# Performance work log

Hardware: AMD Instinct MI355X
Metric: run time of the kernel (lower is better)

## Reference

```python
import jax, jax.numpy as jnp
import numpy as np

EPS = 1e-12
NEG = -1e30


def setup_inputs() -> dict:
    key = jax.random.key(0)
    ks = jax.random.split(key, 7)
    B, Nq, Lp, H, D = 96, 35, 180, 768, 128
    q_hidden = jax.random.normal(ks[0], (B, Nq, H), dtype=jnp.float32)
    pos_hidden = jax.random.normal(ks[1], (B, Lp, H), dtype=jnp.float32)
    neg_hidden = jax.random.normal(ks[2], (B, Lp, H), dtype=jnp.float32)
    W = jax.random.normal(ks[3], (H, D), dtype=jnp.float32) * 0.02
    b = jax.random.normal(ks[4], (D,), dtype=jnp.float32) * 0.02
    # non-punctuation filter mask; guarantee at least one valid token per passage
    pos_mask = jax.random.bernoulli(ks[5], 0.85, (B, Lp)).at[:, 0].set(True)
    neg_mask = jax.random.bernoulli(ks[6], 0.85, (B, Lp)).at[:, 0].set(True)
    return {"q_hidden": q_hidden, "pos_hidden": pos_hidden, "neg_hidden": neg_hidden,
            "W": W, "b": b, "pos_mask": pos_mask, "neg_mask": neg_mask}


def _vector_representation(h, W, b):
    # Linear projection then F.normalize(x) with torch default dim=1,
    # i.e. normalization over the SEQUENCE axis (faithful to source).
    x = jnp.einsum('blh,hd->bld', h, W) + b
    norm = jnp.maximum(jnp.sqrt(jnp.sum(x * x, axis=1, keepdims=True)), EPS)
    return x / norm


def _late_interaction(q, p, mask):
    # q: [Bq, Nq, D], p: [Bp, Lp, D], mask: [Bp, Lp] (True = keep token)
    sim = jnp.einsum('qnd,pld->qpnl', q, p)          # [Bq, Bp, Nq, Lp]
    sim = jnp.where(mask[None, :, None, :], sim, NEG)
    return jnp.max(sim, axis=-1).sum(axis=-1)        # MaxSim: max over Lp, sum over Nq


def reference(q_hidden, pos_hidden, neg_hidden, W, b, pos_mask, neg_mask):
    q = _vector_representation(q_hidden, W, b)
    pos = _vector_representation(pos_hidden, W, b)
    neg = _vector_representation(neg_hidden, W, b)
    pos_scores = _late_interaction(q, pos, pos_mask)
    neg_scores = _late_interaction(q, neg, neg_mask)
    return jnp.concatenate((pos_scores, neg_scores), axis=1)  # [B, 2B]
```

## Files before the change

### kernel.cpp

```cpp
#include <hip/hip_runtime.h>

typedef __attribute__((ext_vector_type(4))) float f32x4;
typedef __attribute__((ext_vector_type(8))) short s16x8;
typedef __attribute__((ext_vector_type(4))) short s16x4;
typedef __bf16 bf16x4 __attribute__((ext_vector_type(4)));

#define B_   96
#define NQ   35
#define LP   180
#define H_   768
#define D_   128
#define NEGF (-1e30f)

#define NROWS 37920
#define QROWS 3360
#define PROWS 17280

__device__ __forceinline__ unsigned short f2bf(float f) {
    return __builtin_bit_cast(unsigned short, (__bf16)f);
}

__device__ __forceinline__ s16x4 cvt_bf4(f32x4 v) {
    return __builtin_bit_cast(s16x4, __builtin_convertvector(v, bf16x4));
}

__device__ __forceinline__ s16x8 pack_bf16(f32x4 v0, f32x4 v1) {
    bf16x4 h0 = __builtin_convertvector(v0, bf16x4);
    bf16x4 h1 = __builtin_convertvector(v1, bf16x4);
    s16x4 a = __builtin_bit_cast(s16x4, h0), b = __builtin_bit_cast(s16x4, h1);
    return __builtin_shufflevector(a, b, 0, 1, 2, 3, 4, 5, 6, 7);
}

__device__ __forceinline__ void glds16(const void* g, void* l) {
    __builtin_amdgcn_global_load_lds(
        (const __attribute__((address_space(1))) unsigned int*)g,
        (__attribute__((address_space(3))) unsigned int*)l,
        16, 0, 0);
}

__device__ __forceinline__ s16x8 ldg16(const unsigned short* sbase, unsigned int voff) {
    s16x8 r;
    asm volatile("global_load_dwordx4 %0, %1, %2"
                 : "=v"(r) : "v"(voff), "s"(sbase));
    return r;
}

#define WAITV(N) do {                                                 \
    asm volatile("s_waitcnt vmcnt(" #N ")" ::: "memory");             \
    __builtin_amdgcn_sched_barrier(0);                                \
} while (0)

#define BAR() do {                                                    \
    __builtin_amdgcn_sched_barrier(0);                                \
    __builtin_amdgcn_s_barrier();                                     \
} while (0)

__global__ __launch_bounds__(256) void prep_k(
    const float* __restrict__ W, unsigned short* __restrict__ wthi,
    const unsigned int* __restrict__ pmask_w, unsigned int* __restrict__ ctrl,
    float* __restrict__ ssq) {
    __shared__ unsigned int rr[256];
    int b = blockIdx.x, t = threadIdx.x;
    if (b < 48) {
        int tid = b * 256 + t;
        int nt = tid / (24 * 64);
        int r = tid - nt * 24 * 64;
        int ks = r / 64, lane = r - ks * 64;
        int m = lane & 15, quad = lane >> 4;
        unsigned short* o = wthi + (size_t)tid * 8;
#pragma unroll
        for (int j = 0; j < 8; j++) {
            int k = ks * 32 + quad * 8 + j;
            o[j] = f2bf(W[(size_t)k * D_ + nt * 16 + m]);
        }
    } else if (b < 192) {
        ssq[(b - 48) * 256 + t] = 0.f;
    } else {
        unsigned int f1 = 0, f3 = 0, f4 = 0;
        for (int w = t; w < 4320; w += 256) {
            unsigned int v = pmask_w[w];
            f1 |= v & 0x0000ff00u;
            f3 |= v & 0xff000000u;
            if (w & 1) f4 |= v & 0x000000ffu;
        }
        rr[t] = f1; __syncthreads();
        for (int s2 = 128; s2; s2 >>= 1) { if (t < s2) rr[t] |= rr[t + s2]; __syncthreads(); }
        if (!t) ctrl[0] = rr[0];
        __syncthreads();
        rr[t] = f3; __syncthreads();
        for (int s2 = 128; s2; s2 >>= 1) { if (t < s2) rr[t] |= rr[t + s2]; __syncthreads(); }
        if (!t) ctrl[1] = rr[0];
        __syncthreads();
        rr[t] = f4; __syncthreads();
        for (int s2 = 128; s2; s2 >>= 1) { if (t < s2) rr[t] |= rr[t + s2]; __syncthreads(); }
        if (!t) ctrl[2] = rr[0];
    }
}

#define STAGE(S) do {                                                                     \
    float* ldw = ld0 + ((S)&3) * 2048;                                                    \
    glds16(gq0 + (S) * 64, ldw);                                                          \
    glds16(gq1 + (S) * 64, ldw + 256);                                                    \
} while (0)

#define LDB(p0, p1, p2, p3, S1) do {                                                      \
    unsigned int k0 = (unsigned int)((S1) * 2048u);                                       \
    p0 = ldg16(wthi, ob0 + k0);                                                           \
    p1 = ldg16(wthi, ob1 + k0);                                                           \
    p2 = ldg16(wthi, ob0 + k0 + 1024u);                                                   \
    p3 = ldg16(wthi, ob1 + k0 + 1024u);                                                   \
} while (0)

#define ACOMP(S, B0, B1, B2, B3) do {                                                     \
    const float* bb = &lds[((S)&3) * 2048];                                               \
    f32x4 l, h;                                                                           \
    l = *(const f32x4*)(bb + rb0 + cA0); h = *(const f32x4*)(bb + rb0 + cA0 + 4);         \
    s16x8 a00 = pack_bf16(l, h);                                                          \
    l = *(const f32x4*)(bb + rb1 + cA0); h = *(const f32x4*)(bb + rb1 + cA0 + 4);         \
    s16x8 a10 = pack_bf16(l, h);                                                          \
    l = *(const f32x4*)(bb + rb0 + cA1); h = *(const f32x4*)(bb + rb0 + cA1 + 4);         \
    s16x8 a01 = pack_bf16(l, h);                                                          \
    l = *(const f32x4*)(bb + rb1 + cA1); h = *(const f32x4*)(bb + rb1 + cA1 + 4);         \
    s16x8 a11 = pack_bf16(l, h);                                                          \
    acc[0][0] = __builtin_amdgcn_mfma_f32_16x16x32_bf16(a00, B0, acc[0][0], 0, 0, 0);     \
    acc[0][1] = __builtin_amdgcn_mfma_f32_16x16x32_bf16(a00, B1, acc[0][1], 0, 0, 0);     \
    acc[1][0] = __builtin_amdgcn_mfma_f32_16x16x32_bf16(a10, B0, acc[1][0], 0, 0, 0);     \
    acc[1][1] = __builtin_amdgcn_mfma_f32_16x16x32_bf16(a10, B1, acc[1][1], 0, 0, 0);     \
    acc[0][0] = __builtin_amdgcn_mfma_f32_16x16x32_bf16(a01, B2, acc[0][0], 0, 0, 0);     \
    acc[0][1] = __builtin_amdgcn_mfma_f32_16x16x32_bf16(a01, B3, acc[0][1], 0, 0, 0);     \
    acc[1][0] = __builtin_amdgcn_mfma_f32_16x16x32_bf16(a11, B2, acc[1][0], 0, 0, 0);     \
    acc[1][1] = __builtin_amdgcn_mfma_f32_16x16x32_bf16(a11, B3, acc[1][1], 0, 0, 0);     \
} while (0)

__global__ __launch_bounds__(256, 4) void proj_k(
    const float* __restrict__ qh, const float* __restrict__ ph, const float* __restrict__ nh,
    const unsigned short* __restrict__ wthi, const float* __restrict__ bias,
    float* __restrict__ x, float* __restrict__ ssq,
    const void* __restrict__ pm, const void* __restrict__ nm,
    const unsigned int* __restrict__ ctrl, unsigned char* __restrict__ maskc) {
    __shared__ float lds[8192];
    int b = blockIdx.x;
    if (b >= 1185) {
        int i = (b - 1185) * 256 + threadIdx.x;
        const void* src = (i < B_ * LP) ? pm : nm;
        int j = (i < B_ * LP) ? i : i - B_ * LP;
        unsigned int c1 = ctrl[0], c3 = ctrl[1], c4 = ctrl[2];
        bool bit;
        if (c1 > 0)       bit = ((const unsigned char*)src)[j] != 0;
        else if (c3 > 0)  bit = ((const float*)src)[j] != 0.0f;
        else if (c4 > 0)  bit = ((const int*)src)[j] != 0;
        else              bit = ((const long long*)src)[j] != 0;
        maskc[i] = bit ? 1 : 0;
        return;
    }
    int t = threadIdx.x;
    int wave = t >> 6, lane = t & 63;
    const float* src; int row0l; int growbase;
    if (b < 105)      { src = qh; row0l = b * 32;         growbase = row0l; }
    else if (b < 645) { src = ph; row0l = (b - 105) * 32; growbase = QROWS + row0l; }
    else              { src = nh; row0l = (b - 645) * 32; growbase = QROWS + PROWS + row0l; }
    int m = lane & 15, quad = lane >> 4;

    int r0 = wave * 8 + (lane >> 4);
    int r1 = r0 + 4;
    int cg0 = (lane & 15) ^ (2 * (r0 & 7));
    int cg1 = (lane & 15) ^ (2 * (r1 & 7));
    const float* gq0 = src + (size_t)(row0l + r0) * H_ + cg0 * 4;
    const float* gq1 = src + (size_t)(row0l + r1) * H_ + cg1 * 4;
    float* ld0 = &lds[wave * 512];

    int nt0 = wave * 2, nt1 = wave * 2 + 1;
    unsigned int ob0 = (unsigned int)(((nt0 * 24) * 64 + lane) * 16);
    unsigned int ob1 = (unsigned int)(((nt1 * 24) * 64 + lane) * 16);

    int swz = 2 * (m & 7);
    int rb0 = m * 64, rb1 = (m + 16) * 64;
    int cA0 = ((quad * 2) ^ swz) * 4;
    int cA1 = ((8 + quad * 2) ^ swz) * 4;

    f32x4 acc[2][2];
#pragma unroll
    for (int mt = 0; mt < 2; mt++)
#pragma unroll
        for (int ntl = 0; ntl < 2; ntl++) acc[mt][ntl] = (f32x4){0.f, 0.f, 0.f, 0.f};

    s16x8 bA0, bA1, bA2, bA3, bB0, bB1, bB2, bB3;

    STAGE(0);
    STAGE(1);
    LDB(bA0, bA1, bA2, bA3, 0);
    STAGE(2);
    WAITV(8);

    BAR(); LDB(bB0, bB1, bB2, bB3, 1);  STAGE(3);  WAITV(8); ACOMP(0,  bA0, bA1, bA2, bA3);
    BAR(); LDB(bA0, bA1, bA2, bA3, 2);  STAGE(4);  WAITV(8); ACOMP(1,  bB0, bB1, bB2, bB3);
    BAR(); LDB(bB0, bB1, bB2, bB3, 3);  STAGE(5);  WAITV(8); ACOMP(2,  bA0, bA1, bA2, bA3);
    BAR(); LDB(bA0, bA1, bA2, bA3, 4);  STAGE(6);  WAITV(8); ACOMP(3,  bB0, bB1, bB2, bB3);
    BAR(); LDB(bB0, bB1, bB2, bB3, 5);  STAGE(7);  WAITV(8); ACOMP(4,  bA0, bA1, bA2, bA3);
    BAR(); LDB(bA0, bA1, bA2, bA3, 6);  STAGE(8);  WAITV(8); ACOMP(5,  bB0, bB1, bB2, bB3);
    BAR(); LDB(bB0, bB1, bB2, bB3, 7);  STAGE(9);  WAITV(8); ACOMP(6,  bA0, bA1, bA2, bA3);
    BAR(); LDB(bA0, bA1, bA2, bA3, 8);  STAGE(10); WAITV(8); ACOMP(7,  bB0, bB1, bB2, bB3);
    BAR(); LDB(bB0, bB1, bB2, bB3, 9);  STAGE(11); WAITV(8); ACOMP(8,  bA0, bA1, bA2, bA3);
    BAR(); LDB(bA0, bA1, bA2, bA3, 10);            WAITV(6); ACOMP(9,  bB0, bB1, bB2, bB3);
    BAR(); LDB(bB0, bB1, bB2, bB3, 11);            WAITV(4); ACOMP(10, bA0, bA1, bA2, bA3);
    BAR();                                         WAITV(0); ACOMP(11, bB0, bB1, bB2, bB3);

#pragma unroll
    for (int mt = 0; mt < 2; mt++) {
        int base = growbase + mt * 16;
        int bk0, bk1, b1start;
        if (base < QROWS)              { bk0 = base / 35;  bk1 = (base + 15) / 35;
                                         b1start = bk1 * 35; }
        else if (base < QROWS + PROWS) { int r0e = base - QROWS;
                                         bk0 = 96 + r0e / 180;  bk1 = 96 + (r0e + 15) / 180;
                                         b1start = QROWS + (bk1 - 96) * 180; }
        else                           { int r0e = base - QROWS - PROWS;
                                         bk0 = 192 + r0e / 180; bk1 = 192 + (r0e + 15) / 180;
                                         b1start = QROWS + PROWS + (bk1 - 192) * 180; }
#pragma unroll
        for (int ntl = 0; ntl < 2; ntl++) {
            int col = (wave * 2 + ntl) * 16 + m;
            float bv = bias[col];
            f32x4 s4 = acc[mt][ntl];
            float slo = 0.f, shi = 0.f;
#pragma unroll
            for (int r = 0; r < 4; r++) {
                int grow = base + quad * 4 + r;
                float v = s4[r] + bv;
                x[(size_t)grow * D_ + col] = v;
                float v2 = v * v;
                if (bk1 > bk0 && grow >= b1start) shi += v2; else slo += v2;
            }
            slo += __shfl_xor(slo, 16); slo += __shfl_xor(slo, 32);
            if (quad == 0) atomicAdd(ssq + (size_t)bk0 * D_ + col, slo);
            if (bk1 > bk0) {
                shi += __shfl_xor(shi, 16); shi += __shfl_xor(shi, 32);
                if (quad == 0) atomicAdd(ssq + (size_t)bk1 * D_ + col, shi);
            }
        }
    }
}

__global__ __launch_bounds__(256) void scatter_k(
    const float* __restrict__ x, const float* __restrict__ ssq,
    const unsigned char* __restrict__ maskc,
    unsigned short* __restrict__ qfrag, unsigned short* __restrict__ pfrag) {
    int c = blockIdx.x * 256 + threadIdx.x;
    int lane = c & 63, ks = (c >> 6) & 3;
    int quad = lane >> 4, mm = lane & 15;
    int d0 = ks * 32 + quad * 8;
    if (c < 61440) {
        int g = c >> 8;
        int mt = g % 5, qp = g / 5;
        int prow = mt * 16 + mm;
        s16x8 outv = (s16x8){0, 0, 0, 0, 0, 0, 0, 0};
        if (prow < 70) {
            int hi = prow >= 35;
            int bq = qp * 2 + hi;
            int l = prow - hi * 35;
            size_t row = (size_t)bq * 35 + l;
            const f32x4* px = (const f32x4*)(x + row * D_ + d0);
            f32x4 v0 = px[0], v1 = px[1];
            const f32x4* pq = (const f32x4*)(ssq + (size_t)bq * D_ + d0);
            f32x4 q0 = pq[0], q1 = pq[1];
            f32x4 r0, r1;
#pragma unroll
            for (int j = 0; j < 4; j++) {
                r0[j] = rsqrtf(fmaxf(q0[j], 1e-24f));
                r1[j] = rsqrtf(fmaxf(q1[j], 1e-24f));
            }
            outv = pack_bf16(v0 * r0, v1 * r1);
        }
        *(s16x8*)(qfrag + (size_t)c * 8) = outv;
    } else {
        int c2 = c - 61440;
        int g = c2 >> 8;
        int nt = g % 12, pbk = g / 12;
        int l = nt * 16 + mm;
        int lsrc = (l < LP && maskc[pbk * LP + l]) ? l : 0;
        size_t row = QROWS + (size_t)pbk * LP + lsrc;
        const f32x4* px = (const f32x4*)(x + row * D_ + d0);
        f32x4 v0 = px[0], v1 = px[1];
        const f32x4* pq = (const f32x4*)(ssq + (size_t)(96 + pbk) * D_ + d0);
        f32x4 q0 = pq[0], q1 = pq[1];
        f32x4 r0, r1;
#pragma unroll
        for (int j = 0; j < 4; j++) {
            r0[j] = rsqrtf(fmaxf(q0[j], 1e-24f));
            r1[j] = rsqrtf(fmaxf(q1[j], 1e-24f));
        }
        *(s16x8*)(pfrag + (size_t)c2 * 8) = pack_bf16(v0 * r0, v1 * r1);
    }
}

__global__ __launch_bounds__(256, 3) void interact_k(
    const unsigned short* __restrict__ qfrag, const unsigned short* __restrict__ pfrag,
    float* __restrict__ out) {
    __shared__ unsigned short plds[24576];
    int wave = threadIdx.x >> 6, lane = threadIdx.x & 63;
    int b = blockIdx.x;
    int xcd = b & 7, i = b >> 3;
    int c = xcd * 24 + (i % 24);
    int qg = i / 24;
    int side = c / 96, pb = c - side * 96;
    int qp = qg * 4 + wave;
    int m = lane & 15, quad = lane >> 4;

    const unsigned short* pbase = pfrag + (size_t)c * 24576;
    const unsigned short* qbase = qfrag + (size_t)qp * 10240;

#pragma unroll
    for (int ntl = 0; ntl < 3; ntl++) {
        int nt = wave * 3 + ntl;
#pragma unroll
        for (int ks = 0; ks < 4; ks++)
            glds16(pbase + ((size_t)(nt * 4 + ks) * 64 + lane) * 8,
                   &plds[(size_t)(nt * 4 + ks) * 512]);
    }

    s16x8 a[5][4];
#pragma unroll
    for (int mt = 0; mt < 5; mt++)
#pragma unroll
        for (int ks = 0; ks < 4; ks++)
            a[mt][ks] = *(const s16x8*)(qbase + ((size_t)(mt * 4 + ks) * 64 + lane) * 8);

    __syncthreads();

    const f32x4 zero4 = (f32x4){0.f, 0.f, 0.f, 0.f};
    float rmax[5][4];
#pragma unroll
    for (int mt = 0; mt < 5; mt++)
#pragma unroll
        for (int rr = 0; rr < 4; rr++) rmax[mt][rr] = NEGF;

    for (int nt = 0; nt < 12; nt++) {
        s16x8 bfr[4];
#pragma unroll
        for (int ks = 0; ks < 4; ks++)
            bfr[ks] = *(const s16x8*)&plds[((size_t)(nt * 4 + ks) * 64 + lane) * 8];
#pragma unroll
        for (int mt = 0; mt < 5; mt++) {
            f32x4 acc = __builtin_amdgcn_mfma_f32_16x16x32_bf16(a[mt][0], bfr[0], zero4, 0, 0, 0);
            acc = __builtin_amdgcn_mfma_f32_16x16x32_bf16(a[mt][1], bfr[1], acc, 0, 0, 0);
            acc = __builtin_amdgcn_mfma_f32_16x16x32_bf16(a[mt][2], bfr[2], acc, 0, 0, 0);
            acc = __builtin_amdgcn_mfma_f32_16x16x32_bf16(a[mt][3], bfr[3], acc, 0, 0, 0);
#pragma unroll
            for (int rr = 0; rr < 4; rr++)
                rmax[mt][rr] = fmaxf(rmax[mt][rr], acc[rr]);
        }
    }

#pragma unroll
    for (int mt = 0; mt < 5; mt++)
#pragma unroll
        for (int rr = 0; rr < 4; rr++) {
            float v = rmax[mt][rr];
            v = fmaxf(v, __shfl_xor(v, 1));
            v = fmaxf(v, __shfl_xor(v, 2));
            v = fmaxf(v, __shfl_xor(v, 4));
            v = fmaxf(v, __shfl_xor(v, 8));
            rmax[mt][rr] = v;
        }
    float s0 = 0.f, s1 = 0.f;
#pragma unroll
    for (int mt = 0; mt < 5; mt++)
#pragma unroll
        for (int rr = 0; rr < 4; rr++) {
            int prow = mt * 16 + quad * 4 + rr;
            float v = rmax[mt][rr];
            if (prow < 35) s0 += v;
            else if (prow < 70) s1 += v;
        }
    s0 += __shfl_xor(s0, 16); s0 += __shfl_xor(s0, 32);
    s1 += __shfl_xor(s1, 16); s1 += __shfl_xor(s1, 32);
    if (lane == 0) {
        int qb0 = qp * 2, qb1 = qp * 2 + 1;
        out[(size_t)qb0 * (2 * B_) + side * B_ + pb] = s0;
        out[(size_t)qb1 * (2 * B_) + side * B_ + pb] = s1;
    }
}

extern "C" void kernel_launch(void* const* d_in, const int* in_sizes, int n_in,
                              void* d_out, int out_size, void* d_ws, size_t ws_size,
                              hipStream_t stream) {
    const float* qh   = (const float*)d_in[0];
    const float* ph   = (const float*)d_in[1];
    const float* nh   = (const float*)d_in[2];
    const float* W    = (const float*)d_in[3];
    const float* bias = (const float*)d_in[4];
    const void* pmask = d_in[5];
    const void* nmask = d_in[6];
    float* out = (float*)d_out;
    char* ws = (char*)d_ws;

    constexpr size_t CTRL_OFF  = 0;
    constexpr size_t WTHI_OFF  = 256;
    constexpr size_t MASKC_OFF = WTHI_OFF + 196608;
    constexpr size_t SSQ_OFF   = 231424;
    constexpr size_t X_OFF     = SSQ_OFF + 147456;
    constexpr size_t QFRAG_OFF = X_OFF + (size_t)NROWS * D_ * 4;
    constexpr size_t PFRAG_OFF = QFRAG_OFF + 983040;

    unsigned int* ctrl     = (unsigned int*)(ws + CTRL_OFF);
    unsigned short* wthi   = (unsigned short*)(ws + WTHI_OFF);
    unsigned char* maskc   = (unsigned char*)(ws + MASKC_OFF);
    float* ssq             = (float*)(ws + SSQ_OFF);
    float* x               = (float*)(ws + X_OFF);
    unsigned short* qfrag  = (unsigned short*)(ws + QFRAG_OFF);
    unsigned short* pfrag  = (unsigned short*)(ws + PFRAG_OFF);

    prep_k<<<193, 256, 0, stream>>>(W, wthi, (const unsigned int*)pmask, ctrl, ssq);
    proj_k<<<1185 + 135, 256, 0, stream>>>(qh, ph, nh, wthi, bias, x, ssq,
                                           pmask, nmask, ctrl, maskc);
    scatter_k<<<2544, 256, 0, stream>>>(x, ssq, maskc, qfrag, pfrag);
    interact_k<<<2304, 256, 0, stream>>>(qfrag, pfrag, out);
}
```

Baseline: 197.5 us.

## Restructure projection GEMM pipeline into two four-stage LDS buffers with fewer barriers

Replaces the per-stage four-slot LDS ring, which needed a barrier every k-step, with two large buffers that each hold four k-stages. The buffers are filled in bulk, and a three-deep register rotation of weight fragments prefetches further ahead. The aim is to cut barrier count from twelve to three and to hide more global latency. In exchange, LDS per block doubles and launch bounds drop to two blocks per CU, which lowers occupancy.

```diff
diff --git a/kernel.cpp b/kernel.cpp
--- a/kernel.cpp
+++ b/kernel.cpp
@@ -97,10 +97,16 @@
     }
 }
 
-#define STAGE(S) do {                                                                     \
-    float* ldw = ld0 + ((S)&3) * 2048;                                                    \
-    glds16(gq0 + (S) * 64, ldw);                                                          \
-    glds16(gq1 + (S) * 64, ldw + 256);                                                    \
+#define STAGEG(BUF, S0) do {                                                              \
+    float* dst = ld0 + (BUF) * 8192;                                                      \
+    glds16(gq0 + ((S0) + 0) * 64, dst);                                                   \
+    glds16(gq1 + ((S0) + 0) * 64, dst + 256);                                             \
+    glds16(gq0 + ((S0) + 1) * 64, dst + 2048);                                            \
+    glds16(gq1 + ((S0) + 1) * 64, dst + 2304);                                            \
+    glds16(gq0 + ((S0) + 2) * 64, dst + 4096);                                            \
+    glds16(gq1 + ((S0) + 2) * 64, dst + 4352);                                            \
+    glds16(gq0 + ((S0) + 3) * 64, dst + 6144);                                            \
+    glds16(gq1 + ((S0) + 3) * 64, dst + 6400);                                            \
 } while (0)
 
 #define LDB(p0, p1, p2, p3, S1) do {                                                      \
@@ -111,8 +117,8 @@
     p3 = ldg16(wthi, ob1 + k0 + 1024u);                                                   \
 } while (0)
 
-#define ACOMP(S, B0, B1, B2, B3) do {                                                     \
-    const float* bb = &lds[((S)&3) * 2048];                                               \
+#define ACOMP(S, BUF, B0, B1, B2, B3) do {                                                \
+    const float* bb = &lds[(BUF) * 8192 + ((S)&3) * 2048];                                \
     f32x4 l, h;                                                                           \
     l = *(const f32x4*)(bb + rb0 + cA0); h = *(const f32x4*)(bb + rb0 + cA0 + 4);         \
     s16x8 a00 = pack_bf16(l, h);                                                          \
@@ -132,13 +138,13 @@
     acc[1][1] = __builtin_amdgcn_mfma_f32_16x16x32_bf16(a11, B3, acc[1][1], 0, 0, 0);     \
 } while (0)
 
-__global__ __launch_bounds__(256, 4) void proj_k(
+__global__ __launch_bounds__(256, 2) void proj_k(
     const float* __restrict__ qh, const float* __restrict__ ph, const float* __restrict__ nh,
     const unsigned short* __restrict__ wthi, const float* __restrict__ bias,
     float* __restrict__ x, float* __restrict__ ssq,
     const void* __restrict__ pm, const void* __restrict__ nm,
     const unsigned int* __restrict__ ctrl, unsigned char* __restrict__ maskc) {
-    __shared__ float lds[8192];
+    __shared__ float lds[16384];
     int b = blockIdx.x;
     if (b >= 1185) {
         int i = (b - 1185) * 256 + threadIdx.x;
@@ -184,26 +190,32 @@
 #pragma unroll
         for (int ntl = 0; ntl < 2; ntl++) acc[mt][ntl] = (f32x4){0.f, 0.f, 0.f, 0.f};
 
-    s16x8 bA0, bA1, bA2, bA3, bB0, bB1, bB2, bB3;
-
-    STAGE(0);
-    STAGE(1);
-    LDB(bA0, bA1, bA2, bA3, 0);
-    STAGE(2);
-    WAITV(8);
-
-    BAR(); LDB(bB0, bB1, bB2, bB3, 1);  STAGE(3);  WAITV(8); ACOMP(0,  bA0, bA1, bA2, bA3);
-    BAR(); LDB(bA0, bA1, bA2, bA3, 2);  STAGE(4);  WAITV(8); ACOMP(1,  bB0, bB1, bB2, bB3);
-    BAR(); LDB(bB0, bB1, bB2, bB3, 3);  STAGE(5);  WAITV(8); ACOMP(2,  bA0, bA1, bA2, bA3);
-    BAR(); LDB(bA0, bA1, bA2, bA3, 4);  STAGE(6);  WAITV(8); ACOMP(3,  bB0, bB1, bB2, bB3);
-    BAR(); LDB(bB0, bB1, bB2, bB3, 5);  STAGE(7);  WAITV(8); ACOMP(4,  bA0, bA1, bA2, bA3);
-    BAR(); LDB(bA0, bA1, bA2, bA3, 6);  STAGE(8);  WAITV(8); ACOMP(5,  bB0, bB1, bB2, bB3);
-    BAR(); LDB(bB0, bB1, bB2, bB3, 7);  STAGE(9);  WAITV(8); ACOMP(6,  bA0, bA1, bA2, bA3);
-    BAR(); LDB(bA0, bA1, bA2, bA3, 8);  STAGE(10); WAITV(8); ACOMP(7,  bB0, bB1, bB2, bB3);
-    BAR(); LDB(bB0, bB1, bB2, bB3, 9);  STAGE(11); WAITV(8); ACOMP(8,  bA0, bA1, bA2, bA3);
-    BAR(); LDB(bA0, bA1, bA2, bA3, 10);            WAITV(6); ACOMP(9,  bB0, bB1, bB2, bB3);
-    BAR(); LDB(bB0, bB1, bB2, bB3, 11);            WAITV(4); ACOMP(10, bA0, bA1, bA2, bA3);
-    BAR();                                         WAITV(0); ACOMP(11, bB0, bB1, bB2, bB3);
+    s16x8 sa0, sa1, sa2, sa3;
+    s16x8 sb0, sb1, sb2, sb3;
+    s16x8 sc0, sc1, sc2, sc3;
+
+    STAGEG(0, 0);
+    LDB(sa0, sa1, sa2, sa3, 0);
+    LDB(sb0, sb1, sb2, sb3, 1);
+    STAGEG(1, 4);
+    LDB(sc0, sc1, sc2, sc3, 2);
+
+    WAITV(16); BAR();
+    ACOMP(0, 0, sa0, sa1, sa2, sa3);
+    LDB(sa0, sa1, sa2, sa3, 3);  WAITV(16); ACOMP(1, 0, sb0, sb1, sb2, sb3);
+    LDB(sb0, sb1, sb2, sb3, 4);  WAITV(8);  ACOMP(2, 0, sc0, sc1, sc2, sc3);
+    LDB(sc0, sc1, sc2, sc3, 5);  WAITV(8);  ACOMP(3, 0, sa0, sa1, sa2, sa3);
+    BAR();
+    STAGEG(0, 8);
+    LDB(sa0, sa1, sa2, sa3, 6);  WAITV(16); ACOMP(4, 1, sb0, sb1, sb2, sb3);
+    LDB(sb0, sb1, sb2, sb3, 7);  WAITV(16); ACOMP(5, 1, sc0, sc1, sc2, sc3);
+    LDB(sc0, sc1, sc2, sc3, 8);  WAITV(8);  ACOMP(6, 1, sa0, sa1, sa2, sa3);
+    LDB(sa0, sa1, sa2, sa3, 9);  WAITV(8);  ACOMP(7, 1, sb0, sb1, sb2, sb3);
+    BAR();
+    LDB(sb0, sb1, sb2, sb3, 10); WAITV(8);  ACOMP(8, 0, sc0, sc1, sc2, sc3);
+    LDB(sc0, sc1, sc2, sc3, 11); WAITV(8);  ACOMP(9, 0, sa0, sa1, sa2, sa3);
+    WAITV(4);  ACOMP(10, 0, sb0, sb1, sb2, sb3);
+    WAITV(0);  ACOMP(11, 0, sc0, sc1, sc2, sc3);
 
 #pragma unroll
     for (int mt = 0; mt < 2; mt++) {
```

After: 197.8 us. Within noise of the previous version (+0.2%).

## Enlarge projection tile to 64 rows with triple-buffered LDS pipeline

Applied to the files above, without the earlier changes.

The projection GEMM now gives each block 64 rows instead of 32, and lets a block span the query, positive and negative inputs through a per-row source selector with a clamped tail. The main aim is to halve the per-row reloads of the bf16 weight fragments from global memory and L2. LDS staging moves from a 4-stage to a 3-stage ring of larger buffers, and B fragments rotate through three register sets. In exchange, per-block LDS use and accumulator registers grow, occupancy drops from 4 to 3 blocks, and the last block is only half full.

```diff
diff --git a/kernel.cpp b/kernel.cpp
--- a/kernel.cpp
+++ b/kernel.cpp
@@ -54,6 +54,16 @@
     __builtin_amdgcn_sched_barrier(0);                                \
     __builtin_amdgcn_s_barrier();                                     \
 } while (0)
+
+__device__ __forceinline__ const float* rowsrc(const float* qh, const float* ph,
+                                               const float* nh, int r, int lane) {
+    int rc = r < (NROWS - 1) ? r : (NROWS - 1);
+    const float* p;
+    if (rc < QROWS)              p = qh + (size_t)rc * H_;
+    else if (rc < QROWS + PROWS) p = ph + (size_t)(rc - QROWS) * H_;
+    else                         p = nh + (size_t)(rc - QROWS - PROWS) * H_;
+    return p + (((lane & 15) ^ (2 * (rc & 7))) << 2);
+}
 
 __global__ __launch_bounds__(256) void prep_k(
     const float* __restrict__ W, unsigned short* __restrict__ wthi,
@@ -97,10 +107,12 @@
     }
 }
 
-#define STAGE(S) do {                                                                     \
-    float* ldw = ld0 + ((S)&3) * 2048;                                                    \
-    glds16(gq0 + (S) * 64, ldw);                                                          \
-    glds16(gq1 + (S) * 64, ldw + 256);                                                    \
+#define STAGE64(S) do {                                                                   \
+    float* dst = &lds[((S) % 3) * 4096 + wave * 1024];                                    \
+    glds16(gq0 + (S) * 64, dst);                                                          \
+    glds16(gq1 + (S) * 64, dst + 256);                                                    \
+    glds16(gq2 + (S) * 64, dst + 512);                                                    \
+    glds16(gq3 + (S) * 64, dst + 768);                                                    \
 } while (0)
 
 #define LDB(p0, p1, p2, p3, S1) do {                                                      \
@@ -111,37 +123,53 @@
     p3 = ldg16(wthi, ob1 + k0 + 1024u);                                                   \
 } while (0)
 
-#define ACOMP(S, B0, B1, B2, B3) do {                                                     \
-    const float* bb = &lds[((S)&3) * 2048];                                               \
-    f32x4 l, h;                                                                           \
-    l = *(const f32x4*)(bb + rb0 + cA0); h = *(const f32x4*)(bb + rb0 + cA0 + 4);         \
-    s16x8 a00 = pack_bf16(l, h);                                                          \
-    l = *(const f32x4*)(bb + rb1 + cA0); h = *(const f32x4*)(bb + rb1 + cA0 + 4);         \
-    s16x8 a10 = pack_bf16(l, h);                                                          \
-    l = *(const f32x4*)(bb + rb0 + cA1); h = *(const f32x4*)(bb + rb0 + cA1 + 4);         \
-    s16x8 a01 = pack_bf16(l, h);                                                          \
-    l = *(const f32x4*)(bb + rb1 + cA1); h = *(const f32x4*)(bb + rb1 + cA1 + 4);         \
-    s16x8 a11 = pack_bf16(l, h);                                                          \
-    acc[0][0] = __builtin_amdgcn_mfma_f32_16x16x32_bf16(a00, B0, acc[0][0], 0, 0, 0);     \
-    acc[0][1] = __builtin_amdgcn_mfma_f32_16x16x32_bf16(a00, B1, acc[0][1], 0, 0, 0);     \
-    acc[1][0] = __builtin_amdgcn_mfma_f32_16x16x32_bf16(a10, B0, acc[1][0], 0, 0, 0);     \
-    acc[1][1] = __builtin_amdgcn_mfma_f32_16x16x32_bf16(a10, B1, acc[1][1], 0, 0, 0);     \
-    acc[0][0] = __builtin_amdgcn_mfma_f32_16x16x32_bf16(a01, B2, acc[0][0], 0, 0, 0);     \
-    acc[0][1] = __builtin_amdgcn_mfma_f32_16x16x32_bf16(a01, B3, acc[0][1], 0, 0, 0);     \
-    acc[1][0] = __builtin_amdgcn_mfma_f32_16x16x32_bf16(a11, B2, acc[1][0], 0, 0, 0);     \
-    acc[1][1] = __builtin_amdgcn_mfma_f32_16x16x32_bf16(a11, B3, acc[1][1], 0, 0, 0);     \
+#define ACOMP64(S, B0, B1, B2, B3) do {                                                   \
+    const float* bb = &lds[((S) % 3) * 4096];                                             \
+    f32x4 l, h; s16x8 a0, a1, a2, a3;                                                     \
+    l = *(const f32x4*)(bb + rbm0 + cA0); h = *(const f32x4*)(bb + rbm0 + cA0 + 4);       \
+    a0 = pack_bf16(l, h);                                                                 \
+    l = *(const f32x4*)(bb + rbm1 + cA0); h = *(const f32x4*)(bb + rbm1 + cA0 + 4);       \
+    a1 = pack_bf16(l, h);                                                                 \
+    l = *(const f32x4*)(bb + rbm2 + cA0); h = *(const f32x4*)(bb + rbm2 + cA0 + 4);       \
+    a2 = pack_bf16(l, h);                                                                 \
+    l = *(const f32x4*)(bb + rbm3 + cA0); h = *(const f32x4*)(bb + rbm3 + cA0 + 4);       \
+    a3 = pack_bf16(l, h);                                                                 \
+    acc[0][0] = __builtin_amdgcn_mfma_f32_16x16x32_bf16(a0, B0, acc[0][0], 0, 0, 0);      \
+    acc[0][1] = __builtin_amdgcn_mfma_f32_16x16x32_bf16(a0, B1, acc[0][1], 0, 0, 0);      \
+    acc[1][0] = __builtin_amdgcn_mfma_f32_16x16x32_bf16(a1, B0, acc[1][0], 0, 0, 0);      \
+    acc[1][1] = __builtin_amdgcn_mfma_f32_16x16x32_bf16(a1, B1, acc[1][1], 0, 0, 0);      \
+    acc[2][0] = __builtin_amdgcn_mfma_f32_16x16x32_bf16(a2, B0, acc[2][0], 0, 0, 0);      \
+    acc[2][1] = __builtin_amdgcn_mfma_f32_16x16x32_bf16(a2, B1, acc[2][1], 0, 0, 0);      \
+    acc[3][0] = __builtin_amdgcn_mfma_f32_16x16x32_bf16(a3, B0, acc[3][0], 0, 0, 0);      \
+    acc[3][1] = __builtin_amdgcn_mfma_f32_16x16x32_bf16(a3, B1, acc[3][1], 0, 0, 0);      \
+    l = *(const f32x4*)(bb + rbm0 + cA1); h = *(const f32x4*)(bb + rbm0 + cA1 + 4);       \
+    a0 = pack_bf16(l, h);                                                                 \
+    l = *(const f32x4*)(bb + rbm1 + cA1); h = *(const f32x4*)(bb + rbm1 + cA1 + 4);       \
+    a1 = pack_bf16(l, h);                                                                 \
+    l = *(const f32x4*)(bb + rbm2 + cA1); h = *(const f32x4*)(bb + rbm2 + cA1 + 4);       \
+    a2 = pack_bf16(l, h);                                                                 \
+    l = *(const f32x4*)(bb + rbm3 + cA1); h = *(const f32x4*)(bb + rbm3 + cA1 + 4);       \
+    a3 = pack_bf16(l, h);                                                                 \
+    acc[0][0] = __builtin_amdgcn_mfma_f32_16x16x32_bf16(a0, B2, acc[0][0], 0, 0, 0);      \
+    acc[0][1] = __builtin_amdgcn_mfma_f32_16x16x32_bf16(a0, B3, acc[0][1], 0, 0, 0);      \
+    acc[1][0] = __builtin_amdgcn_mfma_f32_16x16x32_bf16(a1, B2, acc[1][0], 0, 0, 0);      \
+    acc[1][1] = __builtin_amdgcn_mfma_f32_16x16x32_bf16(a1, B3, acc[1][1], 0, 0, 0);      \
+    acc[2][0] = __builtin_amdgcn_mfma_f32_16x16x32_bf16(a2, B2, acc[2][0], 0, 0, 0);      \
+    acc[2][1] = __builtin_amdgcn_mfma_f32_16x16x32_bf16(a2, B3, acc[2][1], 0, 0, 0);      \
+    acc[3][0] = __builtin_amdgcn_mfma_f32_16x16x32_bf16(a3, B2, acc[3][0], 0, 0, 0);      \
+    acc[3][1] = __builtin_amdgcn_mfma_f32_16x16x32_bf16(a3, B3, acc[3][1], 0, 0, 0);      \
 } while (0)
 
-__global__ __launch_bounds__(256, 4) void proj_k(
+__global__ __launch_bounds__(256, 3) void proj_k(
     const float* __restrict__ qh, const float* __restrict__ ph, const float* __restrict__ nh,
     const unsigned short* __restrict__ wthi, const float* __restrict__ bias,
     float* __restrict__ x, float* __restrict__ ssq,
     const void* __restrict__ pm, const void* __restrict__ nm,
     const unsigned int* __restrict__ ctrl, unsigned char* __restrict__ maskc) {
-    __shared__ float lds[8192];
+    __shared__ float lds[12288];
     int b = blockIdx.x;
-    if (b >= 1185) {
-        int i = (b - 1185) * 256 + threadIdx.x;
+    if (b >= 593) {
+        int i = (b - 593) * 256 + threadIdx.x;
         const void* src = (i < B_ * LP) ? pm : nm;
         int j = (i < B_ * LP) ? i : i - B_ * LP;
         unsigned int c1 = ctrl[0], c3 = ctrl[1], c4 = ctrl[2];
@@ -155,87 +183,83 @@
     }
     int t = threadIdx.x;
     int wave = t >> 6, lane = t & 63;
-    const float* src; int row0l; int growbase;
-    if (b < 105)      { src = qh; row0l = b * 32;         growbase = row0l; }
-    else if (b < 645) { src = ph; row0l = (b - 105) * 32; growbase = QROWS + row0l; }
-    else              { src = nh; row0l = (b - 645) * 32; growbase = QROWS + PROWS + row0l; }
+    int row0 = b * 64;
     int m = lane & 15, quad = lane >> 4;
 
-    int r0 = wave * 8 + (lane >> 4);
-    int r1 = r0 + 4;
-    int cg0 = (lane & 15) ^ (2 * (r0 & 7));
-    int cg1 = (lane & 15) ^ (2 * (r1 & 7));
-    const float* gq0 = src + (size_t)(row0l + r0) * H_ + cg0 * 4;
-    const float* gq1 = src + (size_t)(row0l + r1) * H_ + cg1 * 4;
-    float* ld0 = &lds[wave * 512];
+    int rbase = row0 + wave * 16 + (lane >> 4);
+    const float* gq0 = rowsrc(qh, ph, nh, rbase,      lane);
+    const float* gq1 = rowsrc(qh, ph, nh, rbase + 4,  lane);
+    const float* gq2 = rowsrc(qh, ph, nh, rbase + 8,  lane);
+    const float* gq3 = rowsrc(qh, ph, nh, rbase + 12, lane);
 
     int nt0 = wave * 2, nt1 = wave * 2 + 1;
     unsigned int ob0 = (unsigned int)(((nt0 * 24) * 64 + lane) * 16);
     unsigned int ob1 = (unsigned int)(((nt1 * 24) * 64 + lane) * 16);
 
     int swz = 2 * (m & 7);
-    int rb0 = m * 64, rb1 = (m + 16) * 64;
+    int rbm0 = m * 64, rbm1 = rbm0 + 1024, rbm2 = rbm0 + 2048, rbm3 = rbm0 + 3072;
     int cA0 = ((quad * 2) ^ swz) * 4;
     int cA1 = ((8 + quad * 2) ^ swz) * 4;
 
-    f32x4 acc[2][2];
-#pragma unroll
-    for (int mt = 0; mt < 2; mt++)
+    f32x4 acc[4][2];
+#pragma unroll
+    for (int mt = 0; mt < 4; mt++)
 #pragma unroll
         for (int ntl = 0; ntl < 2; ntl++) acc[mt][ntl] = (f32x4){0.f, 0.f, 0.f, 0.f};
 
-    s16x8 bA0, bA1, bA2, bA3, bB0, bB1, bB2, bB3;
-
-    STAGE(0);
-    STAGE(1);
-    LDB(bA0, bA1, bA2, bA3, 0);
-    STAGE(2);
-    WAITV(8);
-
-    BAR(); LDB(bB0, bB1, bB2, bB3, 1);  STAGE(3);  WAITV(8); ACOMP(0,  bA0, bA1, bA2, bA3);
-    BAR(); LDB(bA0, bA1, bA2, bA3, 2);  STAGE(4);  WAITV(8); ACOMP(1,  bB0, bB1, bB2, bB3);
-    BAR(); LDB(bB0, bB1, bB2, bB3, 3);  STAGE(5);  WAITV(8); ACOMP(2,  bA0, bA1, bA2, bA3);
-    BAR(); LDB(bA0, bA1, bA2, bA3, 4);  STAGE(6);  WAITV(8); ACOMP(3,  bB0, bB1, bB2, bB3);
-    BAR(); LDB(bB0, bB1, bB2, bB3, 5);  STAGE(7);  WAITV(8); ACOMP(4,  bA0, bA1, bA2, bA3);
-    BAR(); LDB(bA0, bA1, bA2, bA3, 6);  STAGE(8);  WAITV(8); ACOMP(5,  bB0, bB1, bB2, bB3);
-    BAR(); LDB(bB0, bB1, bB2, bB3, 7);  STAGE(9);  WAITV(8); ACOMP(6,  bA0, bA1, bA2, bA3);
-    BAR(); LDB(bA0, bA1, bA2, bA3, 8);  STAGE(10); WAITV(8); ACOMP(7,  bB0, bB1, bB2, bB3);
-    BAR(); LDB(bB0, bB1, bB2, bB3, 9);  STAGE(11); WAITV(8); ACOMP(8,  bA0, bA1, bA2, bA3);
-    BAR(); LDB(bA0, bA1, bA2, bA3, 10);            WAITV(6); ACOMP(9,  bB0, bB1, bB2, bB3);
-    BAR(); LDB(bB0, bB1, bB2, bB3, 11);            WAITV(4); ACOMP(10, bA0, bA1, bA2, bA3);
-    BAR();                                         WAITV(0); ACOMP(11, bB0, bB1, bB2, bB3);
-
-#pragma unroll
-    for (int mt = 0; mt < 2; mt++) {
-        int base = growbase + mt * 16;
-        int bk0, bk1, b1start;
-        if (base < QROWS)              { bk0 = base / 35;  bk1 = (base + 15) / 35;
-                                         b1start = bk1 * 35; }
-        else if (base < QROWS + PROWS) { int r0e = base - QROWS;
-                                         bk0 = 96 + r0e / 180;  bk1 = 96 + (r0e + 15) / 180;
-                                         b1start = QROWS + (bk1 - 96) * 180; }
-        else                           { int r0e = base - QROWS - PROWS;
-                                         bk0 = 192 + r0e / 180; bk1 = 192 + (r0e + 15) / 180;
-                                         b1start = QROWS + PROWS + (bk1 - 192) * 180; }
-#pragma unroll
-        for (int ntl = 0; ntl < 2; ntl++) {
-            int col = (wave * 2 + ntl) * 16 + m;
-            float bv = bias[col];
-            f32x4 s4 = acc[mt][ntl];
-            float slo = 0.f, shi = 0.f;
-#pragma unroll
-            for (int r = 0; r < 4; r++) {
-                int grow = base + quad * 4 + r;
-                float v = s4[r] + bv;
-                x[(size_t)grow * D_ + col] = v;
-                float v2 = v * v;
-                if (bk1 > bk0 && grow >= b1start) shi += v2; else slo += v2;
-            }
-            slo += __shfl_xor(slo, 16); slo += __shfl_xor(slo, 32);
-            if (quad == 0) atomicAdd(ssq + (size_t)bk0 * D_ + col, slo);
-            if (bk1 > bk0) {
-                shi += __shfl_xor(shi, 16); shi += __shfl_xor(shi, 32);
-                if (quad == 0) atomicAdd(ssq + (size_t)bk1 * D_ + col, shi);
+    s16x8 sa0, sa1, sa2, sa3;
+    s16x8 sb0, sb1, sb2, sb3;
+    s16x8 sc0, sc1, sc2, sc3;
+
+    STAGE64(0); LDB(sa0, sa1, sa2, sa3, 0);
+    STAGE64(1); LDB(sb0, sb1, sb2, sb3, 1);
+
+    WAITV(8); BAR(); STAGE64(2);  LDB(sc0, sc1, sc2, sc3, 2);  ACOMP64(0,  sa0, sa1, sa2, sa3);
+    WAITV(8); BAR(); STAGE64(3);  LDB(sa0, sa1, sa2, sa3, 3);  ACOMP64(1,  sb0, sb1, sb2, sb3);
+    WAITV(8); BAR(); STAGE64(4);  LDB(sb0, sb1, sb2, sb3, 4);  ACOMP64(2,  sc0, sc1, sc2, sc3);
+    WAITV(8); BAR(); STAGE64(5);  LDB(sc0, sc1, sc2, sc3, 5);  ACOMP64(3,  sa0, sa1, sa2, sa3);
+    WAITV(8); BAR(); STAGE64(6);  LDB(sa0, sa1, sa2, sa3, 6);  ACOMP64(4,  sb0, sb1, sb2, sb3);
+    WAITV(8); BAR(); STAGE64(7);  LDB(sb0, sb1, sb2, sb3, 7);  ACOMP64(5,  sc0, sc1, sc2, sc3);
+    WAITV(8); BAR(); STAGE64(8);  LDB(sc0, sc1, sc2, sc3, 8);  ACOMP64(6,  sa0, sa1, sa2, sa3);
+    WAITV(8); BAR(); STAGE64(9);  LDB(sa0, sa1, sa2, sa3, 9);  ACOMP64(7,  sb0, sb1, sb2, sb3);
+    WAITV(8); BAR(); STAGE64(10); LDB(sb0, sb1, sb2, sb3, 10); ACOMP64(8,  sc0, sc1, sc2, sc3);
+    WAITV(8); BAR(); STAGE64(11); LDB(sc0, sc1, sc2, sc3, 11); ACOMP64(9,  sa0, sa1, sa2, sa3);
+    WAITV(8); BAR();                                           ACOMP64(10, sb0, sb1, sb2, sb3);
+    WAITV(0); BAR();                                           ACOMP64(11, sc0, sc1, sc2, sc3);
+
+#pragma unroll
+    for (int mt = 0; mt < 4; mt++) {
+        int base = row0 + mt * 16;
+        if (base < NROWS) {
+            int bk0, bk1, b1start;
+            if (base < QROWS)              { bk0 = base / 35;  bk1 = (base + 15) / 35;
+                                             b1start = bk1 * 35; }
+            else if (base < QROWS + PROWS) { int r0e = base - QROWS;
+                                             bk0 = 96 + r0e / 180;  bk1 = 96 + (r0e + 15) / 180;
+                                             b1start = QROWS + (bk1 - 96) * 180; }
+            else                           { int r0e = base - QROWS - PROWS;
+                                             bk0 = 192 + r0e / 180; bk1 = 192 + (r0e + 15) / 180;
+                                             b1start = QROWS + PROWS + (bk1 - 192) * 180; }
+#pragma unroll
+            for (int ntl = 0; ntl < 2; ntl++) {
+                int col = (wave * 2 + ntl) * 16 + m;
+                float bv = bias[col];
+                f32x4 s4 = acc[mt][ntl];
+                float slo = 0.f, shi = 0.f;
+#pragma unroll
+                for (int r = 0; r < 4; r++) {
+                    int grow = base + quad * 4 + r;
+                    float v = s4[r] + bv;
+                    x[(size_t)grow * D_ + col] = v;
+                    float v2 = v * v;
+                    if (bk1 > bk0 && grow >= b1start) shi += v2; else slo += v2;
+                }
+                slo += __shfl_xor(slo, 16); slo += __shfl_xor(slo, 32);
+                if (quad == 0) atomicAdd(ssq + (size_t)bk0 * D_ + col, slo);
+                if (bk1 > bk0) {
+                    shi += __shfl_xor(shi, 16); shi += __shfl_xor(shi, 32);
+                    if (quad == 0) atomicAdd(ssq + (size_t)bk1 * D_ + col, shi);
+                }
             }
         }
     }
@@ -411,8 +435,8 @@
     unsigned short* pfrag  = (unsigned short*)(ws + PFRAG_OFF);
 
     prep_k<<<193, 256, 0, stream>>>(W, wthi, (const unsigned int*)pmask, ctrl, ssq);
-    proj_k<<<1185 + 135, 256, 0, stream>>>(qh, ph, nh, wthi, bias, x, ssq,
-                                           pmask, nmask, ctrl, maskc);
+    proj_k<<<593 + 135, 256, 0, stream>>>(qh, ph, nh, wthi, bias, x, ssq,
+                                          pmask, nmask, ctrl, maskc);
     scatter_k<<<2544, 256, 0, stream>>>(x, ssq, maskc, qfrag, pfrag);
     interact_k<<<2304, 256, 0, stream>>>(qfrag, pfrag, out);
 }
```

Result: no change. 200.9 us (+1.7%).
